# Kernel optimization log

Measured on AMD Instinct MI355X. Metric: run time of the kernel, lower is better.

## Reference

```python
import jax, jax.numpy as jnp
import numpy as np

U_NUM, I_NUM, F_DIM, N_EDGES, BATCH = 50000, 20000, 64, 1000000, 131072
T = 1.0  # temperature

def setup_inputs() -> dict:
    key = jax.random.key(0)
    ks = jax.random.split(key, 16)
    return {
        'embed_user': jax.random.normal(ks[0], (U_NUM, F_DIM), jnp.float32) * 0.01,
        'embed_item': jax.random.normal(ks[1], (I_NUM, F_DIM), jnp.float32) * 0.01,
        'old_U_emb': jax.random.normal(ks[2], (U_NUM, F_DIM), jnp.float32),
        'old_I_emb': jax.random.normal(ks[3], (I_NUM, F_DIM), jnp.float32),
        'edge_rows': jax.random.randint(ks[4], (N_EDGES,), 0, U_NUM, jnp.int32),
        'edge_cols': jax.random.randint(ks[5], (N_EDGES,), 0, I_NUM, jnp.int32),
        'ui_vals': jax.random.uniform(ks[6], (N_EDGES,), jnp.float32),
        'iu_vals': jax.random.uniform(ks[7], (N_EDGES,), jnp.float32),
        'user': jax.random.randint(ks[8], (BATCH,), 0, U_NUM, jnp.int32),
        'item_i': jax.random.randint(ks[9], (BATCH,), 0, U_NUM, jnp.int32),
        'item_j': jax.random.randint(ks[10], (BATCH,), 0, U_NUM, jnp.int32),
        'degree_U': jax.random.uniform(ks[11], (BATCH,), jnp.float32),
        'item_z_U': jax.random.randint(ks[12], (BATCH,), 0, U_NUM, jnp.int32),
        'user_': jax.random.randint(ks[13], (BATCH,), 0, I_NUM, jnp.int32),
        'item_i_': jax.random.randint(ks[14], (BATCH,), 0, I_NUM, jnp.int32),
        'item_j_': jax.random.randint(ks[15], (BATCH,), 0, I_NUM, jnp.int32),
        'degree_I': jax.random.uniform(jax.random.fold_in(key, 99), (BATCH,), jnp.float32),
        'item_z_I': jax.random.randint(jax.random.fold_in(key, 98), (BATCH,), 0, I_NUM, jnp.int32),
    }

def _spmm_ui(vals, rows, cols, item_emb):
    # (U x I sparse) @ item_emb -> [U, F]
    return jax.ops.segment_sum(vals[:, None] * item_emb[cols], rows, num_segments=U_NUM)

def _spmm_iu(vals, rows, cols, user_emb):
    # (I x U sparse) @ user_emb -> [I, F]
    return jax.ops.segment_sum(vals[:, None] * user_emb[rows], cols, num_segments=I_NUM)

def _contrastive(idx_u, idx_i, idx_j, degree, num, old_emb, gcn_emb):
    u = old_emb[idx_u]            # [B, F]
    pi = gcn_emb[idx_i]           # [B, F]
    pj = gcn_emb[idx_j]           # [B, F]
    si = jnp.sum(u * pi, axis=-1) / T
    sj = jnp.sum(u * pj, axis=-1) / T
    # -log(exp(si) / (exp(sj) + exp(si))) = logaddexp(si, sj) - si  (stable form)
    log_ratio = si - jnp.logaddexp(si, sj)
    return -jnp.sum(log_ratio * degree) / num

def reference(embed_user, embed_item, old_U_emb, old_I_emb, ui_vals, iu_vals,
              degree_U, degree_I, edge_rows, edge_cols,
              user, item_i, item_j, item_z_U, user_, item_i_, item_j_, item_z_I):
    u0, i0 = embed_user, embed_item
    u1 = _spmm_ui(ui_vals, edge_rows, edge_cols, i0)
    i1 = _spmm_iu(iu_vals, edge_rows, edge_cols, u0)
    u2 = _spmm_ui(ui_vals, edge_rows, edge_cols, i1)
    i2 = _spmm_iu(iu_vals, edge_rows, edge_cols, u1)
    u3 = _spmm_ui(ui_vals, edge_rows, edge_cols, i2)
    i3 = _spmm_iu(iu_vals, edge_rows, edge_cols, u2)
    gcn_u = u0 + 0.5 * u1 + (1.0 / 3.0) * u2 + 0.25 * u3
    gcn_i = i0 + 0.5 * i1 + (1.0 / 3.0) * i2 + 0.25 * i3
    loss = _contrastive(user, item_i, item_j, degree_U, U_NUM, old_U_emb, gcn_u)
    loss = loss + _contrastive(user_, item_i_, item_j_, degree_I, I_NUM, old_I_emb, gcn_i)
    return loss
```

## Files before the change

kernel.cpp:

```cpp
#include <hip/hip_runtime.h>

#define U_NUM 50000
#define I_NUM 20000
#define F_DIM 64
#define N_EDGES 1000000
#define BATCH 131072

#define FP_U 200
#define FP_I 160
#define CAPF_U 5632
#define CAPF_I 6912
#define TILE 8192
#define NBU 123
#define NBI 123
#define CVB 512

#if defined(__has_builtin)
#if __has_builtin(__builtin_amdgcn_cvt_pk_f32_fp8) && __has_builtin(__builtin_amdgcn_cvt_pk_fp8_f32)
#define HW_FP8 1
#endif
#endif

typedef float v2f __attribute__((ext_vector_type(2)));

__device__ __forceinline__ void dec4(unsigned u, float* f) {
#ifdef HW_FP8
    v2f lo = __builtin_amdgcn_cvt_pk_f32_fp8((int)u, false);
    v2f hi = __builtin_amdgcn_cvt_pk_f32_fp8((int)u, true);
    f[0] = lo.x; f[1] = lo.y; f[2] = hi.x; f[3] = hi.y;
#else
    #pragma unroll
    for (int i = 0; i < 4; i++) {
        unsigned v = (u >> (8 * i)) & 0xFFu;
        unsigned s = v >> 7, e = (v >> 3) & 15u, m = v & 7u;
        float mag = (e == 0) ? (float)m * 0.001953125f
                             : __uint_as_float(((e + 120u) << 23) | (m << 20));
        f[i] = s ? -mag : mag;
    }
#endif
}

#ifndef HW_FP8
__device__ __forceinline__ unsigned char enc1(float x) {
    unsigned s = (__float_as_uint(x) >> 31) << 7;
    float a = fabsf(x);
    if (a >= 448.f) return (unsigned char)(s | 0x7E);
    if (a < 0.015625f) {
        int m = __float2int_rn(a * 512.f);
        if (m >= 8) return (unsigned char)(s | 0x08);
        return (unsigned char)(s | m);
    }
    unsigned au = __float_as_uint(a);
    au += 0x7FFFFu + ((au >> 20) & 1u);
    int e = (int)(au >> 23) - 127;
    if (e > 8) return (unsigned char)(s | 0x7E);
    return (unsigned char)(s | ((unsigned)(e + 7) << 3) | ((au >> 20) & 7u));
}
#endif

__device__ __forceinline__ unsigned enc4(float a, float b, float c, float d) {
#ifdef HW_FP8
    int v = __builtin_amdgcn_cvt_pk_fp8_f32(a, b, 0, false);
    v = __builtin_amdgcn_cvt_pk_fp8_f32(c, d, v, true);
    return (unsigned)v;
#else
    return (unsigned)enc1(a) | ((unsigned)enc1(b) << 8)
         | ((unsigned)enc1(c) << 16) | ((unsigned)enc1(d) << 24);
#endif
}

__device__ __forceinline__ unsigned short f2b(float f) {
    unsigned b = __float_as_uint(f);
    b += 0x7FFFu + ((b >> 16) & 1u);
    return (unsigned short)(b >> 16);
}

#define N_EU 800000
#define N_EI 320000
#define N_OU 800000
#define N_OI 320000
#define CVT_TOT (N_EU + N_EI + N_OU + N_OI)
__global__ void build_fine(const int* __restrict__ rows, const int* __restrict__ cols,
                           const float* __restrict__ uiv, const float* __restrict__ iuv,
                           int* __restrict__ fcurU, int2* __restrict__ fbufU,
                           int* __restrict__ fcurI, int2* __restrict__ fbufI,
                           const float* __restrict__ eU, const float* __restrict__ eI,
                           const float* __restrict__ oU, const float* __restrict__ oI,
                           unsigned* __restrict__ e8U, unsigned* __restrict__ e8I,
                           unsigned* __restrict__ o8U, unsigned* __restrict__ o8I)
{
    if (blockIdx.x >= NBU + NBI) {
        for (int idx = (blockIdx.x - NBU - NBI) * 256 + threadIdx.x;
             idx < CVT_TOT; idx += CVB * 256) {
            const float* s; unsigned* d; int off; float sc;
            if (idx < N_EU)                      { s = eU; d = e8U; off = idx; sc = 128.f; }
            else if (idx < N_EU + N_EI)          { s = eI; d = e8I; off = idx - N_EU; sc = 128.f; }
            else if (idx < N_EU + N_EI + N_OU)   { s = oU; d = o8U; off = idx - N_EU - N_EI; sc = 1.f; }
            else                                 { s = oI; d = o8I; off = idx - N_EU - N_EI - N_OU; sc = 1.f; }
            float4 v = ((const float4*)s)[off];
            d[off] = enc4(v.x * sc, v.y * sc, v.z * sc, v.w * sc);
        }
        return;
    }

    __shared__ int2 rec[TILE];
    __shared__ unsigned char pid[TILE];
    __shared__ int hist[256], scan[256], curs[256], delta[256];

    bool isU = blockIdx.x < NBU;
    int tb = isU ? blockIdx.x : blockIdx.x - NBU;
    int n0 = tb * TILE;
    int n  = min(TILE, N_EDGES - n0);
    int bins  = isU ? FP_U : FP_I;
    int capf  = isU ? CAPF_U : CAPF_I;
    int shift = isU ? 8 : 7;
    int* fcur = isU ? fcurU : fcurI;
    int2* fbuf = isU ? fbufU : fbufI;
    const int* keys = isU ? rows : cols;
    const int* srcs = isU ? cols : rows;
    const float* vals = isU ? uiv : iuv;

    hist[threadIdx.x] = 0;
    __syncthreads();

    for (int t = threadIdx.x; t < n; t += 256)
        atomicAdd(&hist[keys[n0 + t] >> shift], 1);
    __syncthreads();

    int v = hist[threadIdx.x];
    scan[threadIdx.x] = v;
    __syncthreads();
    for (int off = 1; off < 256; off <<= 1) {
        int t = ((int)threadIdx.x >= off) ? scan[threadIdx.x - off] : 0;
        __syncthreads();
        scan[threadIdx.x] += t;
        __syncthreads();
    }
    int lbase = scan[threadIdx.x] - v;
    curs[threadIdx.x] = lbase;
    if ((int)threadIdx.x < bins) {
        int res = v ? atomicAdd(&fcur[threadIdx.x], v) : 0;
        delta[threadIdx.x] = threadIdx.x * capf + res - lbase;
    }
    __syncthreads();

    for (int t = threadIdx.x; t < n; t += 256) {
        int key = keys[n0 + t];
        int src = srcs[n0 + t];
        float vv = vals[n0 + t];
        int b = key >> shift;
        int slot = atomicAdd(&curs[b], 1);
        int2 r;
        r.x = (int)(((unsigned)src << 16) | (unsigned)key);
        r.y = __float_as_int(vv);
        rec[slot] = r;
        pid[slot] = (unsigned char)b;
    }
    __syncthreads();

    for (int t = threadIdx.x; t < n; t += 256) {
        int b = pid[t];
        int a = delta[b] + t;
        if (a < (b + 1) * capf) fbuf[a] = rec[t];
    }
}

__global__ void sort_csr(const int* __restrict__ fcurU, const int2* __restrict__ fbufU,
                         int* __restrict__ ptrU, int* __restrict__ cntU, unsigned* __restrict__ edgesU,
                         const int* __restrict__ fcurI, const int2* __restrict__ fbufI,
                         int* __restrict__ ptrI, int* __restrict__ cntI, unsigned* __restrict__ edgesI)
{
    __shared__ int hist[256], scan[256], curs[256];
    __shared__ int gbase_s;

    const int* fcur; const int2* fbuf; int* ptr; int* cnt; unsigned* edges;
    int fp, bins, capf, nrow;
    if (blockIdx.x < FP_U) {
        fcur = fcurU; fbuf = fbufU; ptr = ptrU; cnt = cntU; edges = edgesU;
        fp = blockIdx.x; bins = 256; capf = CAPF_U; nrow = U_NUM;
    } else {
        fcur = fcurI; fbuf = fbufI; ptr = ptrI; cnt = cntI; edges = edgesI;
        fp = blockIdx.x - FP_U; bins = 128; capf = CAPF_I; nrow = I_NUM;
    }

    if (threadIdx.x == 0) gbase_s = 0;
    for (int i = threadIdx.x; i < bins; i += 256) hist[i] = 0;
    __syncthreads();

    int contrib = ((int)threadIdx.x < fp) ? min(fcur[threadIdx.x], capf) : 0;
    #pragma unroll
    for (int off = 32; off > 0; off >>= 1) contrib += __shfl_down(contrib, off, 64);
    if ((threadIdx.x & 63) == 0 && contrib) atomicAdd(&gbase_s, contrib);

    int n = min(fcur[fp], capf);
    const int2* src = fbuf + (size_t)fp * capf;
    int mask = bins - 1;

    for (int t = threadIdx.x; t < n; t += 256) {
        int dst = src[t].x & 0xFFFF;
        atomicAdd(&hist[dst & mask], 1);
    }
    __syncthreads();

    int v = ((int)threadIdx.x < bins) ? hist[threadIdx.x] : 0;
    scan[threadIdx.x] = v;
    __syncthreads();
    for (int off = 1; off < 256; off <<= 1) {
        int t = ((int)threadIdx.x >= off) ? scan[threadIdx.x - off] : 0;
        __syncthreads();
        scan[threadIdx.x] += t;
        __syncthreads();
    }
    int ex = scan[threadIdx.x] - v;
    curs[threadIdx.x] = ex;
    __syncthreads();
    int gbase = gbase_s;

    if ((int)threadIdx.x < bins) {
        int row = fp * bins + threadIdx.x;
        if (row < nrow) {
            ptr[row] = gbase + ex;
            cnt[row] = v;
        }
    }

    for (int t = threadIdx.x; t < n; t += 256) {
        int2 r = src[t];
        int dst = r.x & 0xFFFF;
        int pos = atomicAdd(&curs[dst & mask], 1);
        unsigned rec = ((unsigned)f2b(__int_as_float(r.y)) << 16)
                     | ((unsigned)r.x >> 16);
        edges[gbase + pos] = rec;
    }
}

template <int MODE>
__global__ void spmm_level(const int* __restrict__ ptrU, const int* __restrict__ cntU,
                           const unsigned* __restrict__ edgesU, const unsigned* __restrict__ srcU,
                           unsigned* __restrict__ dstU,
                           const unsigned* __restrict__ l0U, const unsigned* __restrict__ l1U,
                           const unsigned* __restrict__ l2U, unsigned* __restrict__ g8U,
                           const int* __restrict__ ptrI, const int* __restrict__ cntI,
                           const unsigned* __restrict__ edgesI, const unsigned* __restrict__ srcI,
                           unsigned* __restrict__ dstI,
                           const unsigned* __restrict__ l0I, const unsigned* __restrict__ l1I,
                           const unsigned* __restrict__ l2I, unsigned* __restrict__ g8I)
{
    int wave = (blockIdx.x * blockDim.x + threadIdx.x) >> 6;
    bool isU = wave < U_NUM;
    int row = isU ? wave : wave - U_NUM;
    if (!isU && row >= I_NUM) return;

    const int*  ptr   = isU ? ptrU   : ptrI;
    const int*  cnt   = isU ? cntU   : cntI;
    const unsigned* edges = isU ? edgesU : edgesI;
    const unsigned* semb  = isU ? srcU   : srcI;

    int lane = threadIdx.x & 63;
    int sub  = lane >> 4;
    int q    = lane & 15;
    int begin = __builtin_amdgcn_readfirstlane(ptr[row]);
    int len   = __builtin_amdgcn_readfirstlane(cnt[row]);
    const unsigned* erow = edges + begin;

    float4 a0 = make_float4(0.f, 0.f, 0.f, 0.f);
    float4 a1 = make_float4(0.f, 0.f, 0.f, 0.f);
    float4 a2 = make_float4(0.f, 0.f, 0.f, 0.f);
    float4 a3 = make_float4(0.f, 0.f, 0.f, 0.f);
    int k = sub;
    for (; k + 12 < len; k += 16) {
        unsigned r0 = erow[k];
        unsigned r1 = erow[k + 4];
        unsigned r2 = erow[k + 8];
        unsigned r3 = erow[k + 12];
        unsigned x0 = semb[((size_t)(r0 & 0xFFFFu) << 4) + q];
        unsigned x1 = semb[((size_t)(r1 & 0xFFFFu) << 4) + q];
        unsigned x2 = semb[((size_t)(r2 & 0xFFFFu) << 4) + q];
        unsigned x3 = semb[((size_t)(r3 & 0xFFFFu) << 4) + q];
        float v0 = __uint_as_float(r0 & 0xFFFF0000u);
        float v1 = __uint_as_float(r1 & 0xFFFF0000u);
        float v2 = __uint_as_float(r2 & 0xFFFF0000u);
        float v3 = __uint_as_float(r3 & 0xFFFF0000u);
        float f0[4], f1[4], f2[4], f3[4];
        dec4(x0, f0); dec4(x1, f1); dec4(x2, f2); dec4(x3, f3);
        a0.x += v0 * f0[0]; a0.y += v0 * f0[1]; a0.z += v0 * f0[2]; a0.w += v0 * f0[3];
        a1.x += v1 * f1[0]; a1.y += v1 * f1[1]; a1.z += v1 * f1[2]; a1.w += v1 * f1[3];
        a2.x += v2 * f2[0]; a2.y += v2 * f2[1]; a2.z += v2 * f2[2]; a2.w += v2 * f2[3];
        a3.x += v3 * f3[0]; a3.y += v3 * f3[1]; a3.z += v3 * f3[2]; a3.w += v3 * f3[3];
    }
    for (; k < len; k += 4) {
        unsigned r0 = erow[k];
        unsigned x0 = semb[((size_t)(r0 & 0xFFFFu) << 4) + q];
        float v0 = __uint_as_float(r0 & 0xFFFF0000u);
        float f0[4];
        dec4(x0, f0);
        a0.x += v0 * f0[0]; a0.y += v0 * f0[1]; a0.z += v0 * f0[2]; a0.w += v0 * f0[3];
    }
    float4 acc;
    acc.x = (a0.x + a1.x) + (a2.x + a3.x);
    acc.y = (a0.y + a1.y) + (a2.y + a3.y);
    acc.z = (a0.z + a1.z) + (a2.z + a3.z);
    acc.w = (a0.w + a1.w) + (a2.w + a3.w);

    acc.x += __shfl_xor(acc.x, 16, 64);
    acc.y += __shfl_xor(acc.y, 16, 64);
    acc.z += __shfl_xor(acc.z, 16, 64);
    acc.w += __shfl_xor(acc.w, 16, 64);
    acc.x += __shfl_xor(acc.x, 32, 64);
    acc.y += __shfl_xor(acc.y, 32, 64);
    acc.z += __shfl_xor(acc.z, 32, 64);
    acc.w += __shfl_xor(acc.w, 32, 64);

    if (sub == 0) {
        size_t ro = ((size_t)row << 4) + q;
        if (MODE < 2) {
            unsigned* dst = isU ? dstU : dstI;
            dst[ro] = enc4(acc.x, acc.y, acc.z, acc.w);
        } else {
            const unsigned* l0 = isU ? l0U : l0I;
            const unsigned* l1 = isU ? l1U : l1I;
            const unsigned* l2 = isU ? l2U : l2I;
            unsigned* g8       = isU ? g8U : g8I;
            float e[4], b[4], c[4];
            dec4(l0[ro], e); dec4(l1[ro], b); dec4(l2[ro], c);
            const float third = 1.f / 3.f;
            float gx = 0.125f * (e[0] + 0.5f * b[0] + third * c[0] + 0.25f * acc.x);
            float gy = 0.125f * (e[1] + 0.5f * b[1] + third * c[1] + 0.25f * acc.y);
            float gz = 0.125f * (e[2] + 0.5f * b[2] + third * c[2] + 0.25f * acc.z);
            float gw = 0.125f * (e[3] + 0.5f * b[3] + third * c[3] + 0.25f * acc.w);
            g8[ro] = enc4(gx, gy, gz, gw);
        }
    }
}

__device__ __forceinline__ float dotq(const float* a, const float* b) {
    return a[0] * b[0] + a[1] * b[1] + a[2] * b[2] + a[3] * b[3];
}

__global__ void __launch_bounds__(256, 2)
contrastive_both(const unsigned* __restrict__ oldU, const unsigned* __restrict__ gcnU,
                 const int* __restrict__ userU, const int* __restrict__ iiU,
                 const int* __restrict__ ijU, const float* __restrict__ degU,
                 const unsigned* __restrict__ oldI, const unsigned* __restrict__ gcnI,
                 const int* __restrict__ userI, const int* __restrict__ iiI,
                 const int* __restrict__ ijI, const float* __restrict__ degI,
                 float* __restrict__ out)
{
    int lane = threadIdx.x & 63;
    int sub  = lane >> 4;
    int ql   = lane & 15;
    int qg = (blockIdx.x * blockDim.x + threadIdx.x) >> 4;
    int s0 = qg << 2;

    int sel = ql >> 2, so = s0 + (ql & 3);
    const int* pu = (sel == 0) ? (userU + so) : (sel == 1) ? (iiU + so)
                  : (sel == 2) ? (ijU + so)   : ((const int*)degU + so);
    const int* pi = (sel == 0) ? (userI + so) : (sel == 1) ? (iiI + so)
                  : (sel == 2) ? (ijI + so)   : ((const int*)degI + so);
    int idxU = *pu;
    int idxI = *pi;

    int qb = sub << 4;
    unsigned Au[4], Ai[4], Aj[4], Bu[4], Bi[4], Bj[4];
    #pragma unroll
    for (int t = 0; t < 4; t++) {
        int uU = __shfl(idxU, qb + t, 64);
        int iU = __shfl(idxU, qb + 4 + t, 64);
        int jU = __shfl(idxU, qb + 8 + t, 64);
        int uI = __shfl(idxI, qb + t, 64);
        int iI = __shfl(idxI, qb + 4 + t, 64);
        int jI = __shfl(idxI, qb + 8 + t, 64);
        Au[t] = oldU[((size_t)uU << 4) + ql];
        Ai[t] = gcnU[((size_t)iU << 4) + ql];
        Aj[t] = gcnU[((size_t)jU << 4) + ql];
        Bu[t] = oldI[((size_t)uI << 4) + ql];
        Bi[t] = gcnI[((size_t)iI << 4) + ql];
        Bj[t] = gcnI[((size_t)jI << 4) + ql];
    }

    float siU[4], sjU[4], siI[4], sjI[4];
    #pragma unroll
    for (int t = 0; t < 4; t++) {
        float fu[4], fi[4], fj[4];
        dec4(Au[t], fu); dec4(Ai[t], fi); dec4(Aj[t], fj);
        siU[t] = dotq(fu, fi); sjU[t] = dotq(fu, fj);
        dec4(Bu[t], fu); dec4(Bi[t], fi); dec4(Bj[t], fj);
        siI[t] = dotq(fu, fi); sjI[t] = dotq(fu, fj);
    }

    #pragma unroll
    for (int off = 1; off < 16; off <<= 1) {
        #pragma unroll
        for (int t = 0; t < 4; t++) {
            siU[t] += __shfl_xor(siU[t], off, 64);
            sjU[t] += __shfl_xor(sjU[t], off, 64);
            siI[t] += __shfl_xor(siI[t], off, 64);
            sjI[t] += __shfl_xor(sjI[t], off, 64);
        }
    }

    int t3 = ql & 3;
    bool isI = (ql & 4) != 0;
    float si = isI ? siI[t3] : siU[t3];
    float sj = isI ? sjI[t3] : sjU[t3];
    float dg = __int_as_float(__shfl(isI ? idxI : idxU, qb + 12 + t3, 64));
    float inv = isI ? (1.f / I_NUM) : (1.f / U_NUM);

    const float S = 0.0625f;
    si *= S; sj *= S;
    float m = fmaxf(si, sj);
    float lse = m + logf(expf(si - m) + expf(sj - m));
    float acc = (ql < 8) ? -(si - lse) * dg * inv : 0.f;

    #pragma unroll
    for (int off = 32; off > 0; off >>= 1) acc += __shfl_down(acc, off, 64);
    __shared__ float wsum[4];
    if (lane == 0) wsum[threadIdx.x >> 6] = acc;
    __syncthreads();
    if (threadIdx.x == 0)
        atomicAdd(out, wsum[0] + wsum[1] + wsum[2] + wsum[3]);
}

extern "C" void kernel_launch(void* const* d_in, const int* in_sizes, int n_in,
                              void* d_out, int out_size, void* d_ws, size_t ws_size,
                              hipStream_t stream)
{
    const float* embed_user = (const float*)d_in[0];
    const float* embed_item = (const float*)d_in[1];
    const float* old_U      = (const float*)d_in[2];
    const float* old_I      = (const float*)d_in[3];
    const int*   erow       = (const int*)d_in[4];
    const int*   ecol       = (const int*)d_in[5];
    const float* ui_vals    = (const float*)d_in[6];
    const float* iu_vals    = (const float*)d_in[7];
    const int*   user       = (const int*)d_in[8];
    const int*   item_i     = (const int*)d_in[9];
    const int*   item_j     = (const int*)d_in[10];
    const float* degU       = (const float*)d_in[11];
    const int*   user_      = (const int*)d_in[13];
    const int*   item_i_    = (const int*)d_in[14];
    const int*   item_j_    = (const int*)d_in[15];
    const float* degI       = (const float*)d_in[16];

    const size_t UF = (size_t)U_NUM * F_DIM;
    const size_t IF = (size_t)I_NUM * F_DIM;
    const size_t FRECU = (size_t)FP_U * CAPF_U;
    const size_t FRECI = (size_t)FP_I * CAPF_I;

    int2*  fbufU  = (int2*)d_ws;
    int2*  fbufI  = fbufU + FRECU;
    unsigned* edgesU = (unsigned*)(fbufI + FRECI);
    unsigned* edgesI = edgesU + N_EDGES;
    char* cur = (char*)(edgesI + N_EDGES);
    unsigned* e8U = (unsigned*)cur; cur += UF;
    unsigned* e8I = (unsigned*)cur; cur += IF;
    unsigned* o8U = (unsigned*)cur; cur += UF;
    unsigned* o8I = (unsigned*)cur; cur += IF;
    unsigned* u1_8 = (unsigned*)cur; cur += UF;
    unsigned* u2_8 = (unsigned*)cur; cur += UF;
    unsigned* i1_8 = (unsigned*)cur; cur += IF;
    unsigned* i2_8 = (unsigned*)cur; cur += IF;
    unsigned* g8U  = (unsigned*)cur; cur += UF;
    unsigned* g8I  = (unsigned*)cur; cur += IF;
    int* fcurU = (int*)cur;
    int* fcurI = fcurU + 256;
    int* ptrU  = fcurI + 256;
    int* cntUa = ptrU + U_NUM;
    int* ptrI  = cntUa + U_NUM;
    int* cntIa = ptrI + I_NUM;

    dim3 blk(256);
    const int bf_blocks  = NBU + NBI + CVB;
    const int st_blocks  = FP_U + FP_I;
    const int spmm_blocks = (U_NUM + I_NUM) / 4;

    hipMemsetAsync(fcurU, 0, 512 * sizeof(int), stream);
    hipMemsetAsync(d_out, 0, sizeof(float), stream);

    build_fine<<<bf_blocks, blk, 0, stream>>>(erow, ecol, ui_vals, iu_vals,
                                              fcurU, fbufU, fcurI, fbufI,
                                              embed_user, embed_item, old_U, old_I,
                                              e8U, e8I, o8U, o8I);
    sort_csr<<<st_blocks, blk, 0, stream>>>(fcurU, fbufU, ptrU, cntUa, edgesU,
                                            fcurI, fbufI, ptrI, cntIa, edgesI);

    spmm_level<0><<<spmm_blocks, blk, 0, stream>>>(
        ptrU, cntUa, edgesU, e8I, u1_8, nullptr, nullptr, nullptr, nullptr,
        ptrI, cntIa, edgesI, e8U, i1_8, nullptr, nullptr, nullptr, nullptr);
    spmm_level<1><<<spmm_blocks, blk, 0, stream>>>(
        ptrU, cntUa, edgesU, i1_8, u2_8, nullptr, nullptr, nullptr, nullptr,
        ptrI, cntIa, edgesI, u1_8, i2_8, nullptr, nullptr, nullptr, nullptr);
    spmm_level<2><<<spmm_blocks, blk, 0, stream>>>(
        ptrU, cntUa, edgesU, i2_8, nullptr, e8U, u1_8, u2_8, g8U,
        ptrI, cntIa, edgesI, u2_8, nullptr, e8I, i1_8, i2_8, g8I);

    contrastive_both<<<2048, blk, 0, stream>>>(o8U, g8U, user, item_i, item_j, degU,
                                               o8I, g8I, user_, item_i_, item_j_, degI,
                                               (float*)d_out);
}
```

Measured before the change: 301.3 us.

## Remap SpMM wave lanes to 16 edges x 4 uint4 feature quarters

Changes the per-row SpMM gather so each wave handles 16 edges at once, with each lane loading a 16-byte uint4 slice (16 fp8 features) instead of a 4-byte word over 4 edges. The aim is fewer, wider gather loads and more edges in flight per iteration, with row outputs and layer combines written as uint4 stores. In exchange each lane holds 16 accumulators, which raises register pressure. It also needs a 4-step cross-lane shuffle reduction over 16 values, and the tail loop issues gathers for padding edges with value zero.

```diff
diff --git a/kernel.cpp b/kernel.cpp
--- a/kernel.cpp
+++ b/kernel.cpp
@@ -254,81 +254,88 @@
     const int*  ptr   = isU ? ptrU   : ptrI;
     const int*  cnt   = isU ? cntU   : cntI;
     const unsigned* edges = isU ? edgesU : edgesI;
-    const unsigned* semb  = isU ? srcU   : srcI;
+    const uint4* semb4 = (const uint4*)(isU ? srcU : srcI);
 
     int lane = threadIdx.x & 63;
-    int sub  = lane >> 4;
-    int q    = lane & 15;
+    int g = lane & 15;
+    int s = lane >> 4;
     int begin = __builtin_amdgcn_readfirstlane(ptr[row]);
     int len   = __builtin_amdgcn_readfirstlane(cnt[row]);
     const unsigned* erow = edges + begin;
 
-    float4 a0 = make_float4(0.f, 0.f, 0.f, 0.f);
-    float4 a1 = make_float4(0.f, 0.f, 0.f, 0.f);
-    float4 a2 = make_float4(0.f, 0.f, 0.f, 0.f);
-    float4 a3 = make_float4(0.f, 0.f, 0.f, 0.f);
-    int k = sub;
-    for (; k + 12 < len; k += 16) {
-        unsigned r0 = erow[k];
-        unsigned r1 = erow[k + 4];
-        unsigned r2 = erow[k + 8];
-        unsigned r3 = erow[k + 12];
-        unsigned x0 = semb[((size_t)(r0 & 0xFFFFu) << 4) + q];
-        unsigned x1 = semb[((size_t)(r1 & 0xFFFFu) << 4) + q];
-        unsigned x2 = semb[((size_t)(r2 & 0xFFFFu) << 4) + q];
-        unsigned x3 = semb[((size_t)(r3 & 0xFFFFu) << 4) + q];
-        float v0 = __uint_as_float(r0 & 0xFFFF0000u);
-        float v1 = __uint_as_float(r1 & 0xFFFF0000u);
-        float v2 = __uint_as_float(r2 & 0xFFFF0000u);
-        float v3 = __uint_as_float(r3 & 0xFFFF0000u);
-        float f0[4], f1[4], f2[4], f3[4];
-        dec4(x0, f0); dec4(x1, f1); dec4(x2, f2); dec4(x3, f3);
-        a0.x += v0 * f0[0]; a0.y += v0 * f0[1]; a0.z += v0 * f0[2]; a0.w += v0 * f0[3];
-        a1.x += v1 * f1[0]; a1.y += v1 * f1[1]; a1.z += v1 * f1[2]; a1.w += v1 * f1[3];
-        a2.x += v2 * f2[0]; a2.y += v2 * f2[1]; a2.z += v2 * f2[2]; a2.w += v2 * f2[3];
-        a3.x += v3 * f3[0]; a3.y += v3 * f3[1]; a3.z += v3 * f3[2]; a3.w += v3 * f3[3];
-    }
-    for (; k < len; k += 4) {
-        unsigned r0 = erow[k];
-        unsigned x0 = semb[((size_t)(r0 & 0xFFFFu) << 4) + q];
-        float v0 = __uint_as_float(r0 & 0xFFFF0000u);
-        float f0[4];
-        dec4(x0, f0);
-        a0.x += v0 * f0[0]; a0.y += v0 * f0[1]; a0.z += v0 * f0[2]; a0.w += v0 * f0[3];
-    }
-    float4 acc;
-    acc.x = (a0.x + a1.x) + (a2.x + a3.x);
-    acc.y = (a0.y + a1.y) + (a2.y + a3.y);
-    acc.z = (a0.z + a1.z) + (a2.z + a3.z);
-    acc.w = (a0.w + a1.w) + (a2.w + a3.w);
-
-    acc.x += __shfl_xor(acc.x, 16, 64);
-    acc.y += __shfl_xor(acc.y, 16, 64);
-    acc.z += __shfl_xor(acc.z, 16, 64);
-    acc.w += __shfl_xor(acc.w, 16, 64);
-    acc.x += __shfl_xor(acc.x, 32, 64);
-    acc.y += __shfl_xor(acc.y, 32, 64);
-    acc.z += __shfl_xor(acc.z, 32, 64);
-    acc.w += __shfl_xor(acc.w, 32, 64);
-
-    if (sub == 0) {
-        size_t ro = ((size_t)row << 4) + q;
+    float acc[16];
+    #pragma unroll
+    for (int j = 0; j < 16; j++) acc[j] = 0.f;
+
+    int k = 0;
+    for (; k + 32 <= len; k += 32) {
+        unsigned ra = erow[k + g];
+        unsigned rb = erow[k + 16 + g];
+        uint4 xa = semb4[((size_t)(ra & 0xFFFFu) << 2) + s];
+        uint4 xb = semb4[((size_t)(rb & 0xFFFFu) << 2) + s];
+        float va = __uint_as_float(ra & 0xFFFF0000u);
+        float vb = __uint_as_float(rb & 0xFFFF0000u);
+        float fa[16], fb[16];
+        dec4(xa.x, fa);     dec4(xa.y, fa + 4);
+        dec4(xa.z, fa + 8); dec4(xa.w, fa + 12);
+        dec4(xb.x, fb);     dec4(xb.y, fb + 4);
+        dec4(xb.z, fb + 8); dec4(xb.w, fb + 12);
+        #pragma unroll
+        for (int j = 0; j < 16; j++) acc[j] += va * fa[j];
+        #pragma unroll
+        for (int j = 0; j < 16; j++) acc[j] += vb * fb[j];
+    }
+    for (; k < len; k += 16) {
+        unsigned ra = (k + g < len) ? erow[k + g] : 0u;
+        uint4 xa = semb4[((size_t)(ra & 0xFFFFu) << 2) + s];
+        float va = __uint_as_float(ra & 0xFFFF0000u);
+        float fa[16];
+        dec4(xa.x, fa);     dec4(xa.y, fa + 4);
+        dec4(xa.z, fa + 8); dec4(xa.w, fa + 12);
+        #pragma unroll
+        for (int j = 0; j < 16; j++) acc[j] += va * fa[j];
+    }
+
+    #pragma unroll
+    for (int off = 1; off < 16; off <<= 1) {
+        #pragma unroll
+        for (int j = 0; j < 16; j++)
+            acc[j] += __shfl_xor(acc[j], off, 64);
+    }
+
+    if (g == 0) {
+        size_t ro = ((size_t)row << 4) + (s << 2);
         if (MODE < 2) {
             unsigned* dst = isU ? dstU : dstI;
-            dst[ro] = enc4(acc.x, acc.y, acc.z, acc.w);
+            uint4 o;
+            o.x = enc4(acc[0],  acc[1],  acc[2],  acc[3]);
+            o.y = enc4(acc[4],  acc[5],  acc[6],  acc[7]);
+            o.z = enc4(acc[8],  acc[9],  acc[10], acc[11]);
+            o.w = enc4(acc[12], acc[13], acc[14], acc[15]);
+            *(uint4*)(dst + ro) = o;
         } else {
             const unsigned* l0 = isU ? l0U : l0I;
             const unsigned* l1 = isU ? l1U : l1I;
             const unsigned* l2 = isU ? l2U : l2I;
             unsigned* g8       = isU ? g8U : g8I;
-            float e[4], b[4], c[4];
-            dec4(l0[ro], e); dec4(l1[ro], b); dec4(l2[ro], c);
+            uint4 e4 = *(const uint4*)(l0 + ro);
+            uint4 b4 = *(const uint4*)(l1 + ro);
+            uint4 c4 = *(const uint4*)(l2 + ro);
+            float e[16], b[16], c[16];
+            dec4(e4.x, e);     dec4(e4.y, e + 4);  dec4(e4.z, e + 8);  dec4(e4.w, e + 12);
+            dec4(b4.x, b);     dec4(b4.y, b + 4);  dec4(b4.z, b + 8);  dec4(b4.w, b + 12);
+            dec4(c4.x, c);     dec4(c4.y, c + 4);  dec4(c4.z, c + 8);  dec4(c4.w, c + 12);
             const float third = 1.f / 3.f;
-            float gx = 0.125f * (e[0] + 0.5f * b[0] + third * c[0] + 0.25f * acc.x);
-            float gy = 0.125f * (e[1] + 0.5f * b[1] + third * c[1] + 0.25f * acc.y);
-            float gz = 0.125f * (e[2] + 0.5f * b[2] + third * c[2] + 0.25f * acc.z);
-            float gw = 0.125f * (e[3] + 0.5f * b[3] + third * c[3] + 0.25f * acc.w);
-            g8[ro] = enc4(gx, gy, gz, gw);
+            float gg[16];
+            #pragma unroll
+            for (int j = 0; j < 16; j++)
+                gg[j] = 0.125f * (e[j] + 0.5f * b[j] + third * c[j] + 0.25f * acc[j]);
+            uint4 o;
+            o.x = enc4(gg[0],  gg[1],  gg[2],  gg[3]);
+            o.y = enc4(gg[4],  gg[5],  gg[6],  gg[7]);
+            o.z = enc4(gg[8],  gg[9],  gg[10], gg[11]);
+            o.w = enc4(gg[12], gg[13], gg[14], gg[15]);
+            *(uint4*)(g8 + ro) = o;
         }
     }
 }
```

Result: slower. 347.1 us (+15.2%).
